# Kernel tuning notes

Hardware: AMD Instinct MI355X
Metric: run time of the kernel (lower is better)

Reference implementation:

```python
import jax, jax.numpy as jnp
import numpy as np

NUM_INDICES = 16
INPUT_DIM = 512
UNITS = 512
BATCH = 1024


def setup_inputs() -> dict:
    key = jax.random.key(0)
    k_x, k_idx, k_w = jax.random.split(key, 3)
    x = jax.random.normal(k_x, (BATCH, INPUT_DIM), dtype=jnp.float32)
    index = jax.random.randint(k_idx, (BATCH,), 0, NUM_INDICES, dtype=jnp.int64)
    # glorot_uniform for kernel, zeros for bias (as in the keras layer)
    limit = np.sqrt(6.0 / (INPUT_DIM + UNITS)).astype(np.float32)
    ws = jax.random.uniform(k_w, (NUM_INDICES, INPUT_DIM, UNITS), dtype=jnp.float32,
                            minval=-limit, maxval=limit)
    bs = jnp.zeros((NUM_INDICES, UNITS), dtype=jnp.float32)
    return {"x": x, "index": index, "ws": ws, "bs": bs}


def reference(x, index, ws, bs):
    # Per-sample expert gather: (B, INPUT_DIM, UNITS) and (B, UNITS)
    w = ws[index]
    b = bs[index]
    # Batched matvec + bias, then relu activation
    out = jnp.einsum('bi,biu->bu', x, w) + b
    return jax.nn.relu(out)
```

## Files before the change

kernel.cpp:

```cpp
#include <hip/hip_runtime.h>

#define BATCH 1024
#define KDIM 512
#define NDIM 512
#define NEXP 16
#define BM 64
#define BN 64
#define BKW 64
#define XLDK 72
#define WLDK 72
#define MAXMT 2
#define NTHR 512

typedef __attribute__((ext_vector_type(8))) short bf16x8;
typedef __attribute__((ext_vector_type(4))) float f32x4;
typedef __attribute__((ext_vector_type(2))) unsigned u32x2;

__device__ __forceinline__ unsigned cvt2(float a, float b) {
    unsigned r;
    asm("v_cvt_pk_bf16_f32 %0, %1, %2" : "=v"(r) : "v"(a), "v"(b));
    return r;
}

#define BAR()                                              \
    do {                                                   \
        asm volatile("s_waitcnt lgkmcnt(0)" ::: "memory"); \
        __builtin_amdgcn_s_barrier();                      \
        asm volatile("" ::: "memory");                     \
    } while (0)

__global__ __launch_bounds__(NTHR) void fused_gemm_kernel(
        const float* __restrict__ x, const int* __restrict__ idx32,
        const float* __restrict__ w, const float* __restrict__ bias,
        float* __restrict__ out) {
    __shared__ int ids[BM];
    __shared__ int wsum[8];
    __shared__ __align__(16) short Xs[2][BM][XLDK];
    __shared__ __align__(16) short Wt[2][BN][WLDK];

    const int t = threadIdx.x;
    const int lane = t & 63, wid = t >> 6;
    const int e = blockIdx.x & (NEXP - 1);
    const int m0 = (blockIdx.x >> 4) * BM;
    const int u0 = blockIdx.y * BN;

    const int wn4 = (t & 15) * 4;
    const int wq = t >> 4;
    const float* wp = w + (size_t)e * KDIM * NDIM + u0 + wn4;
    float4 wA0 = *(const float4*)(wp + (size_t)(2 * wq) * NDIM);
    float4 wA1 = *(const float4*)(wp + (size_t)(2 * wq + 1) * NDIM);
    float4 wB0 = *(const float4*)(wp + (size_t)(BKW + 2 * wq) * NDIM);
    float4 wB1 = *(const float4*)(wp + (size_t)(BKW + 2 * wq + 1) * NDIM);

    int e0, e1;
    {
        int4 dv = ((const int4*)idx32)[lane];
        int2 iv32 = ((const int2*)idx32)[t];
        const bool is32 = __ballot((dv.y | dv.w) != 0) != 0ULL;
        if (is32) {
            e0 = iv32.x;
            e1 = iv32.y;
        } else {
            int4 iv = ((const int4*)idx32)[t];
            e0 = iv.x;
            e1 = iv.z;
        }
    }
    if (t < BM) ids[t] = -1;

    int c = (e0 == e) + (e1 == e);
    int pre = c;
#pragma unroll
    for (int d = 1; d < 64; d <<= 1) {
        int v = __shfl_up(pre, d, 64);
        if (lane >= d) pre += v;
    }
    if (lane == 63) wsum[wid] = pre;
    BAR();
    int cnt_e = 0;
#pragma unroll
    for (int wv = 0; wv < 8; wv++) cnt_e += wsum[wv];
    if (m0 >= cnt_e) return;
    int run = pre - c;
#pragma unroll
    for (int wv = 0; wv < 8; wv++)
        if (wv < wid) run += wsum[wv];
    const int b0 = 2 * t;
    if (e0 == e) {
        unsigned rr = (unsigned)(run - m0);
        if (rr < BM) ids[rr] = b0;
        run++;
    }
    if (e1 == e) {
        unsigned rr = (unsigned)(run - m0);
        if (rr < BM) ids[rr] = b0 + 1;
    }
    BAR();

    const int xr = t >> 3;
    const int xk4 = (t & 7) * 4;
    const int xrow = ids[xr];
    const float* xp = x + (size_t)(xrow < 0 ? 0 : xrow) * KDIM;
    float4 xA0 = *(const float4*)(xp + xk4);
    float4 xA1 = *(const float4*)(xp + xk4 + 32);
    float4 xB0 = *(const float4*)(xp + BKW + xk4);
    float4 xB1 = *(const float4*)(xp + BKW + xk4 + 32);

    const int ml = lane & 15;
    const int kb = (lane >> 4) * 8;
    const int wm = wid >> 2;
    const int wn_ = wid & 3;
    const int am0 = wm * 32 + ml;
    const int nb = wn_ * 16 + ml;

    f32x4 acc0 = {}, acc1 = {};

#define BODY(BUF, IT, XV0, XV1, WV0, WV1)                                     \
    {                                                                         \
        u32x2 hx0, hx1;                                                       \
        hx0[0] = cvt2(XV0.x, XV0.y); hx0[1] = cvt2(XV0.z, XV0.w);             \
        hx1[0] = cvt2(XV1.x, XV1.y); hx1[1] = cvt2(XV1.z, XV1.w);             \
        *(u32x2*)&Xs[BUF][xr][xk4] = hx0;                                     \
        *(u32x2*)&Xs[BUF][xr][xk4 + 32] = hx1;                                \
        *(unsigned*)&Wt[BUF][wn4 + 0][2 * wq] = cvt2(WV0.x, WV1.x);           \
        *(unsigned*)&Wt[BUF][wn4 + 1][2 * wq] = cvt2(WV0.y, WV1.y);           \
        *(unsigned*)&Wt[BUF][wn4 + 2][2 * wq] = cvt2(WV0.z, WV1.z);           \
        *(unsigned*)&Wt[BUF][wn4 + 3][2 * wq] = cvt2(WV0.w, WV1.w);           \
        if ((IT) + 2 < KDIM / BKW) {                                          \
            const int kn = ((IT) + 2) * BKW;                                  \
            XV0 = *(const float4*)(xp + kn + xk4);                            \
            XV1 = *(const float4*)(xp + kn + xk4 + 32);                       \
            WV0 = *(const float4*)(wp + (size_t)(kn + 2 * wq) * NDIM);        \
            WV1 = *(const float4*)(wp + (size_t)(kn + 2 * wq + 1) * NDIM);    \
        }                                                                     \
        BAR();                                                                \
        {                                                                     \
            bf16x8 a0 = *(const bf16x8*)&Xs[BUF][am0][kb];                    \
            bf16x8 a1 = *(const bf16x8*)&Xs[BUF][am0 + 16][kb];               \
            bf16x8 bb = *(const bf16x8*)&Wt[BUF][nb][kb];                     \
            acc0 = __builtin_amdgcn_mfma_f32_16x16x32_bf16(a0, bb, acc0, 0, 0, 0); \
            acc1 = __builtin_amdgcn_mfma_f32_16x16x32_bf16(a1, bb, acc1, 0, 0, 0); \
            bf16x8 a2 = *(const bf16x8*)&Xs[BUF][am0][32 + kb];               \
            bf16x8 a3 = *(const bf16x8*)&Xs[BUF][am0 + 16][32 + kb];          \
            bf16x8 bc = *(const bf16x8*)&Wt[BUF][nb][32 + kb];                \
            acc0 = __builtin_amdgcn_mfma_f32_16x16x32_bf16(a2, bc, acc0, 0, 0, 0); \
            acc1 = __builtin_amdgcn_mfma_f32_16x16x32_bf16(a3, bc, acc1, 0, 0, 0); \
        }                                                                     \
    }

    BODY(0, 0, xA0, xA1, wA0, wA1)
    BODY(1, 1, xB0, xB1, wB0, wB1)
    BODY(0, 2, xA0, xA1, wA0, wA1)
    BODY(1, 3, xB0, xB1, wB0, wB1)
    BODY(0, 4, xA0, xA1, wA0, wA1)
    BODY(1, 5, xB0, xB1, wB0, wB1)
    BODY(0, 6, xA0, xA1, wA0, wA1)
    BODY(1, 7, xB0, xB1, wB0, wB1)
#undef BODY

    const int row4 = (lane >> 4) * 4;
    const float bv = bias[(size_t)e * NDIM + u0 + nb];
#pragma unroll
    for (int r = 0; r < 4; r++) {
        const int orow = ids[wm * 32 + row4 + r];
        if (orow >= 0)
            out[(size_t)orow * NDIM + u0 + nb] = fmaxf(acc0[r] + bv, 0.f);
    }
#pragma unroll
    for (int r = 0; r < 4; r++) {
        const int orow = ids[wm * 32 + 16 + row4 + r];
        if (orow >= 0)
            out[(size_t)orow * NDIM + u0 + nb] = fmaxf(acc1[r] + bv, 0.f);
    }
}

extern "C" void kernel_launch(void* const* d_in, const int* in_sizes, int n_in,
                              void* d_out, int out_size, void* d_ws, size_t ws_size,
                              hipStream_t stream) {
    const float* x = (const float*)d_in[0];
    const int* idx = (const int*)d_in[1];
    const float* w = (const float*)d_in[2];
    const float* bias = (const float*)d_in[3];
    float* out = (float*)d_out;

    fused_gemm_kernel<<<dim3(NEXP * MAXMT, NDIM / BN), NTHR, 0, stream>>>(
        x, idx, w, bias, out);
}
```

Measured before the change: 12.89 us.

## Use one 128-row tile per expert with narrower N and deeper K steps

Each expert is now covered by a single 128-row M tile instead of up to two 64-row tiles. N tiles shrink to 32 columns so the grid still has 256 blocks, and the K step grows to 128, which halves the number of barrier-separated iterations. The aim is to read each expert's weight slice only once, since the second M tile previously re-read W whenever an expert had more than 64 rows, and to cut synchronization overhead. The cost is wasted MFMA work on padded rows when an expert has far fewer than 128 samples, and every block now does the full load and compute with no early exit.

```diff
diff --git a/kernel.cpp b/kernel.cpp
--- a/kernel.cpp
+++ b/kernel.cpp
@@ -4,17 +4,15 @@
 #define KDIM 512
 #define NDIM 512
 #define NEXP 16
-#define BM 64
-#define BN 64
-#define BKW 64
-#define XLDK 72
-#define WLDK 72
-#define MAXMT 2
+#define BM 128
+#define BN 32
+#define BK 128
+#define XLDK 136
+#define WLDK 136
 #define NTHR 512
 
 typedef __attribute__((ext_vector_type(8))) short bf16x8;
 typedef __attribute__((ext_vector_type(4))) float f32x4;
-typedef __attribute__((ext_vector_type(2))) unsigned u32x2;
 
 __device__ __forceinline__ unsigned cvt2(float a, float b) {
     unsigned r;
@@ -40,17 +38,16 @@
 
     const int t = threadIdx.x;
     const int lane = t & 63, wid = t >> 6;
-    const int e = blockIdx.x & (NEXP - 1);
-    const int m0 = (blockIdx.x >> 4) * BM;
+    const int e = blockIdx.x;
     const int u0 = blockIdx.y * BN;
 
-    const int wn4 = (t & 15) * 4;
-    const int wq = t >> 4;
+    const int wn4 = (t & 7) * 4;
+    const int wq = t >> 3;
     const float* wp = w + (size_t)e * KDIM * NDIM + u0 + wn4;
-    float4 wA0 = *(const float4*)(wp + (size_t)(2 * wq) * NDIM);
-    float4 wA1 = *(const float4*)(wp + (size_t)(2 * wq + 1) * NDIM);
-    float4 wB0 = *(const float4*)(wp + (size_t)(BKW + 2 * wq) * NDIM);
-    float4 wB1 = *(const float4*)(wp + (size_t)(BKW + 2 * wq + 1) * NDIM);
+    float4 wA0 = *(const float4*)(wp + (size_t)(0 * BK + 2 * wq) * NDIM);
+    float4 wA1 = *(const float4*)(wp + (size_t)(0 * BK + 2 * wq + 1) * NDIM);
+    float4 wB0 = *(const float4*)(wp + (size_t)(1 * BK + 2 * wq) * NDIM);
+    float4 wB1 = *(const float4*)(wp + (size_t)(1 * BK + 2 * wq + 1) * NDIM);
 
     int e0, e1;
     {
@@ -77,86 +74,84 @@
     }
     if (lane == 63) wsum[wid] = pre;
     BAR();
-    int cnt_e = 0;
-#pragma unroll
-    for (int wv = 0; wv < 8; wv++) cnt_e += wsum[wv];
-    if (m0 >= cnt_e) return;
     int run = pre - c;
 #pragma unroll
     for (int wv = 0; wv < 8; wv++)
         if (wv < wid) run += wsum[wv];
     const int b0 = 2 * t;
     if (e0 == e) {
-        unsigned rr = (unsigned)(run - m0);
-        if (rr < BM) ids[rr] = b0;
+        if ((unsigned)run < BM) ids[run] = b0;
         run++;
     }
     if (e1 == e) {
-        unsigned rr = (unsigned)(run - m0);
-        if (rr < BM) ids[rr] = b0 + 1;
+        if ((unsigned)run < BM) ids[run] = b0 + 1;
     }
     BAR();
 
-    const int xr = t >> 3;
-    const int xk4 = (t & 7) * 4;
+    const int xr = t >> 2;
+    const int xq8 = (t & 3) * 8;
     const int xrow = ids[xr];
     const float* xp = x + (size_t)(xrow < 0 ? 0 : xrow) * KDIM;
-    float4 xA0 = *(const float4*)(xp + xk4);
-    float4 xA1 = *(const float4*)(xp + xk4 + 32);
-    float4 xB0 = *(const float4*)(xp + BKW + xk4);
-    float4 xB1 = *(const float4*)(xp + BKW + xk4 + 32);
+    float4 xA[8], xB[8];
+#pragma unroll
+    for (int j = 0; j < 4; j++) {
+        xA[2 * j]     = *(const float4*)(xp + 0 * BK + xq8 + 32 * j);
+        xA[2 * j + 1] = *(const float4*)(xp + 0 * BK + xq8 + 32 * j + 4);
+        xB[2 * j]     = *(const float4*)(xp + 1 * BK + xq8 + 32 * j);
+        xB[2 * j + 1] = *(const float4*)(xp + 1 * BK + xq8 + 32 * j + 4);
+    }
 
     const int ml = lane & 15;
     const int kb = (lane >> 4) * 8;
-    const int wm = wid >> 2;
-    const int wn_ = wid & 3;
+    const int wm = wid >> 1;
+    const int wn_ = wid & 1;
     const int am0 = wm * 32 + ml;
     const int nb = wn_ * 16 + ml;
 
     f32x4 acc0 = {}, acc1 = {};
 
-#define BODY(BUF, IT, XV0, XV1, WV0, WV1)                                     \
+#define STEP(BUF, S, XV, W0, W1)                                              \
     {                                                                         \
-        u32x2 hx0, hx1;                                                       \
-        hx0[0] = cvt2(XV0.x, XV0.y); hx0[1] = cvt2(XV0.z, XV0.w);             \
-        hx1[0] = cvt2(XV1.x, XV1.y); hx1[1] = cvt2(XV1.z, XV1.w);             \
-        *(u32x2*)&Xs[BUF][xr][xk4] = hx0;                                     \
-        *(u32x2*)&Xs[BUF][xr][xk4 + 32] = hx1;                                \
-        *(unsigned*)&Wt[BUF][wn4 + 0][2 * wq] = cvt2(WV0.x, WV1.x);           \
-        *(unsigned*)&Wt[BUF][wn4 + 1][2 * wq] = cvt2(WV0.y, WV1.y);           \
-        *(unsigned*)&Wt[BUF][wn4 + 2][2 * wq] = cvt2(WV0.z, WV1.z);           \
-        *(unsigned*)&Wt[BUF][wn4 + 3][2 * wq] = cvt2(WV0.w, WV1.w);           \
-        if ((IT) + 2 < KDIM / BKW) {                                          \
-            const int kn = ((IT) + 2) * BKW;                                  \
-            XV0 = *(const float4*)(xp + kn + xk4);                            \
-            XV1 = *(const float4*)(xp + kn + xk4 + 32);                       \
-            WV0 = *(const float4*)(wp + (size_t)(kn + 2 * wq) * NDIM);        \
-            WV1 = *(const float4*)(wp + (size_t)(kn + 2 * wq + 1) * NDIM);    \
+        _Pragma("unroll")                                                     \
+        for (int j = 0; j < 4; j++) {                                         \
+            union { unsigned u[4]; bf16x8 h; } hx;                            \
+            hx.u[0] = cvt2(XV[2 * j].x, XV[2 * j].y);                         \
+            hx.u[1] = cvt2(XV[2 * j].z, XV[2 * j].w);                         \
+            hx.u[2] = cvt2(XV[2 * j + 1].x, XV[2 * j + 1].y);                 \
+            hx.u[3] = cvt2(XV[2 * j + 1].z, XV[2 * j + 1].w);                 \
+            *(bf16x8*)&Xs[BUF][xr][xq8 + 32 * j] = hx.h;                      \
+        }                                                                     \
+        *(unsigned*)&Wt[BUF][wn4 + 0][2 * wq] = cvt2(W0.x, W1.x);             \
+        *(unsigned*)&Wt[BUF][wn4 + 1][2 * wq] = cvt2(W0.y, W1.y);             \
+        *(unsigned*)&Wt[BUF][wn4 + 2][2 * wq] = cvt2(W0.z, W1.z);             \
+        *(unsigned*)&Wt[BUF][wn4 + 3][2 * wq] = cvt2(W0.w, W1.w);             \
+        if ((S) + 2 < KDIM / BK) {                                            \
+            const int kn = ((S) + 2) * BK;                                    \
+            _Pragma("unroll")                                                 \
+            for (int j = 0; j < 4; j++) {                                     \
+                XV[2 * j]     = *(const float4*)(xp + kn + xq8 + 32 * j);     \
+                XV[2 * j + 1] = *(const float4*)(xp + kn + xq8 + 32 * j + 4); \
+            }                                                                 \
+            W0 = *(const float4*)(wp + (size_t)(kn + 2 * wq) * NDIM);         \
+            W1 = *(const float4*)(wp + (size_t)(kn + 2 * wq + 1) * NDIM);     \
         }                                                                     \
         BAR();                                                                \
-        {                                                                     \
-            bf16x8 a0 = *(const bf16x8*)&Xs[BUF][am0][kb];                    \
-            bf16x8 a1 = *(const bf16x8*)&Xs[BUF][am0 + 16][kb];               \
-            bf16x8 bb = *(const bf16x8*)&Wt[BUF][nb][kb];                     \
+        _Pragma("unroll")                                                     \
+        for (int kw = 0; kw < 4; kw++) {                                      \
+            const int k0 = kw * 32;                                           \
+            bf16x8 a0 = *(const bf16x8*)&Xs[BUF][am0][k0 + kb];               \
+            bf16x8 a1 = *(const bf16x8*)&Xs[BUF][am0 + 16][k0 + kb];          \
+            bf16x8 bb = *(const bf16x8*)&Wt[BUF][nb][k0 + kb];                \
             acc0 = __builtin_amdgcn_mfma_f32_16x16x32_bf16(a0, bb, acc0, 0, 0, 0); \
             acc1 = __builtin_amdgcn_mfma_f32_16x16x32_bf16(a1, bb, acc1, 0, 0, 0); \
-            bf16x8 a2 = *(const bf16x8*)&Xs[BUF][am0][32 + kb];               \
-            bf16x8 a3 = *(const bf16x8*)&Xs[BUF][am0 + 16][32 + kb];          \
-            bf16x8 bc = *(const bf16x8*)&Wt[BUF][nb][32 + kb];                \
-            acc0 = __builtin_amdgcn_mfma_f32_16x16x32_bf16(a2, bc, acc0, 0, 0, 0); \
-            acc1 = __builtin_amdgcn_mfma_f32_16x16x32_bf16(a3, bc, acc1, 0, 0, 0); \
         }                                                                     \
     }
 
-    BODY(0, 0, xA0, xA1, wA0, wA1)
-    BODY(1, 1, xB0, xB1, wB0, wB1)
-    BODY(0, 2, xA0, xA1, wA0, wA1)
-    BODY(1, 3, xB0, xB1, wB0, wB1)
-    BODY(0, 4, xA0, xA1, wA0, wA1)
-    BODY(1, 5, xB0, xB1, wB0, wB1)
-    BODY(0, 6, xA0, xA1, wA0, wA1)
-    BODY(1, 7, xB0, xB1, wB0, wB1)
-#undef BODY
+    STEP(0, 0, xA, wA0, wA1)
+    STEP(1, 1, xB, wB0, wB1)
+    STEP(0, 2, xA, wA0, wA1)
+    STEP(1, 3, xB, wB0, wB1)
+#undef STEP
 
     const int row4 = (lane >> 4) * 4;
     const float bv = bias[(size_t)e * NDIM + u0 + nb];
@@ -183,6 +178,6 @@
     const float* bias = (const float*)d_in[3];
     float* out = (float*)d_out;
 
-    fused_gemm_kernel<<<dim3(NEXP * MAXMT, NDIM / BN), NTHR, 0, stream>>>(
+    fused_gemm_kernel<<<dim3(NEXP, NDIM / BN), NTHR, 0, stream>>>(
         x, idx, w, bias, out);
 }
```

Result: no change. 12.77 us (-1.0%).
